# Performance work log

Measured on AMD Instinct MI355X. Metric: run time of the kernel, lower is better.

## Reference

```python
import jax, jax.numpy as jnp
import numpy as np

B, C, H, W = 8, 64, 256, 256
SQ = 256  # max(int(64*16*0.25),1)

def setup_inputs() -> dict:
    key = jax.random.key(0)
    k1, k2, k3, k4, k5 = jax.random.split(key, 5)
    t = jax.random.normal(k1, (B, C, H, W), dtype=jnp.float32)
    reduce_w = jax.random.normal(k2, (SQ, 16 * C), dtype=jnp.float32) * (1.0 / np.sqrt(16 * C))
    reduce_b = jax.random.normal(k3, (SQ,), dtype=jnp.float32) * 0.01
    expand_w = jax.random.normal(k4, (16 * C, SQ), dtype=jnp.float32) * (1.0 / np.sqrt(SQ))
    expand_b = jax.random.normal(k5, (16 * C,), dtype=jnp.float32) * 0.01
    return {"t": t, "reduce_w": reduce_w, "reduce_b": reduce_b,
            "expand_w": expand_w, "expand_b": expand_b}

def _mish(x):
    return x * jnp.tanh(jax.nn.softplus(x))

def reference(t, reduce_w, reduce_b, expand_w, expand_b):
    b, c, h, w = t.shape  # h, w assumed multiples of 4 (no pad needed)
    gh, gw = h // 4, w // 4
    # split into 4x4 grid of patches: [B, C, 4, gh, 4, gw]
    tg = t.reshape(b, c, 4, gh, 4, gw)
    # global avg pool per patch -> [B, C, 4, 4]; reorder to cat order (i*4+j)*C + c
    pooled = tg.mean(axis=(3, 5))                      # [B, C, 4, 4]
    pooled = pooled.transpose(0, 2, 3, 1).reshape(b, 16 * c)  # [B, 16C]
    # squeeze-excite MLP (1x1 convs on [B,16C,1,1] == linear layers)
    s = _mish(pooled @ reduce_w.T + reduce_b)          # [B, SQ]
    g = jax.nn.sigmoid(s @ expand_w.T + expand_b)      # [B, 16C]
    # gates back to grid: [B, 4, 4, C] -> [B, C, 4, 1, 4, 1]
    gates = g.reshape(b, 4, 4, c).transpose(0, 3, 1, 2)[:, :, :, None, :, None]
    out = (tg * gates).reshape(b, c, h, w)
    return out
```

## Files before the change

kernel.cpp:

```cpp
#include <hip/hip_runtime.h>
#include <math.h>


#define Bsz 8
#define Csz 64
#define Hsz 256
#define Wsz 256
#define SQsz 256
#define C16 1024

typedef float f32x4 __attribute__((ext_vector_type(4)));

__global__ __launch_bounds__(256) void pool_kernel(const float* __restrict__ t,
                                                   float* __restrict__ pooled) {
    int bid = blockIdx.x;
    int p   = bid & 15;
    int bc  = bid >> 4;
    int i   = p >> 2, j = p & 3;
    const float* base = t + (((size_t)bc * Hsz + (size_t)i * 64) * Wsz + (size_t)j * 64);
    int tid = threadIdx.x;
    float sum = 0.f;
#pragma unroll
    for (int k = 0; k < 4; ++k) {
        int g    = tid + k * 256;
        int row  = g >> 4;
        int col4 = g & 15;
        f32x4 v = *(const f32x4*)(base + (size_t)row * Wsz + col4 * 4);
        sum += v.x + v.y + v.z + v.w;
    }
#pragma unroll
    for (int off = 32; off > 0; off >>= 1) sum += __shfl_down(sum, off, 64);
    __shared__ float wsum[4];
    if ((tid & 63) == 0) wsum[tid >> 6] = sum;
    __syncthreads();
    if (tid == 0) {
        float s = wsum[0] + wsum[1] + wsum[2] + wsum[3];
        int b = bc >> 6;
        int c = bc & 63;
        pooled[b * C16 + p * Csz + c] = s * (1.0f / 4096.0f);
    }
}

__global__ __launch_bounds__(1024) void reduce_kernel(const float* __restrict__ pooled,
                                                      const float* __restrict__ reduce_w,
                                                      const float* __restrict__ reduce_b,
                                                      float* __restrict__ s_out) {
    int o   = blockIdx.x;
    int tid = threadIdx.x;
    int w   = tid >> 6;
    int l   = tid & 63;
    float wv = reduce_w[(size_t)o * C16 + tid];
    float acc[Bsz];
#pragma unroll
    for (int b = 0; b < Bsz; ++b)
        acc[b] = wv * pooled[b * C16 + tid];
#pragma unroll
    for (int off = 32; off > 0; off >>= 1) {
#pragma unroll
        for (int b = 0; b < Bsz; ++b)
            acc[b] += __shfl_xor(acc[b], off, 64);
    }
    __shared__ float red[16][Bsz];
    if (l == 0) {
#pragma unroll
        for (int b = 0; b < Bsz; ++b) red[w][b] = acc[b];
    }
    __syncthreads();
    if (tid < Bsz) {
        float x = reduce_b[o];
#pragma unroll
        for (int q = 0; q < 16; ++q) x += red[q][tid];
        float sp = (x > 15.f) ? x : log1pf(expf(x));
        s_out[tid * SQsz + o] = x * tanhf(sp);
    }
}

__global__ __launch_bounds__(256) void expand_kernel(const float* __restrict__ s_in,
                                                     const float* __restrict__ expand_w,
                                                     const float* __restrict__ expand_b,
                                                     float* __restrict__ g_out) {
    int o   = blockIdx.x;
    int tid = threadIdx.x;
    int w   = tid >> 6;
    int l   = tid & 63;
    float wv = expand_w[(size_t)o * SQsz + tid];
    float acc[Bsz];
#pragma unroll
    for (int b = 0; b < Bsz; ++b)
        acc[b] = wv * s_in[b * SQsz + tid];
#pragma unroll
    for (int off = 32; off > 0; off >>= 1) {
#pragma unroll
        for (int b = 0; b < Bsz; ++b)
            acc[b] += __shfl_xor(acc[b], off, 64);
    }
    __shared__ float red[4][Bsz];
    if (l == 0) {
#pragma unroll
        for (int b = 0; b < Bsz; ++b) red[w][b] = acc[b];
    }
    __syncthreads();
    if (tid < Bsz) {
        float x = expand_b[o] + red[0][tid] + red[1][tid] + red[2][tid] + red[3][tid];
        g_out[tid * C16 + o] = 1.0f / (1.0f + expf(-x));
    }
}

__global__ __launch_bounds__(256) void scale_kernel(const float* __restrict__ t,
                                                    const float* __restrict__ g,
                                                    float* __restrict__ out) {
    unsigned int idx = blockIdx.x * 256u + threadIdx.x;
    int w4 = idx & 63;
    int h  = (idx >> 6) & 255;
    int c  = (idx >> 14) & 63;
    int b  = idx >> 20;
    int p  = ((h >> 6) << 2) | (w4 >> 4);
    float gate = g[(b << 10) + (p << 6) + c];
    f32x4 v = __builtin_nontemporal_load((const f32x4*)(t + (size_t)idx * 4));
    f32x4 r;
    r.x = v.x * gate;
    r.y = v.y * gate;
    r.z = v.z * gate;
    r.w = v.w * gate;
    __builtin_nontemporal_store(r, (f32x4*)(out + (size_t)idx * 4));
}

extern "C" void kernel_launch(void* const* d_in, const int* in_sizes, int n_in,
                              void* d_out, int out_size, void* d_ws, size_t ws_size,
                              hipStream_t stream) {
    const float* t        = (const float*)d_in[0];
    const float* reduce_w = (const float*)d_in[1];
    const float* reduce_b = (const float*)d_in[2];
    const float* expand_w = (const float*)d_in[3];
    const float* expand_b = (const float*)d_in[4];
    float* out = (float*)d_out;

    float* pooled = (float*)d_ws;
    float* s_buf  = pooled + Bsz * C16;
    float* g_buf  = s_buf + Bsz * SQsz;

    pool_kernel  <<<Bsz * Csz * 16, 256, 0, stream>>>(t, pooled);
    reduce_kernel<<<SQsz,          1024, 0, stream>>>(pooled, reduce_w, reduce_b, s_buf);
    expand_kernel<<<C16,            256, 0, stream>>>(s_buf, expand_w, expand_b, g_buf);
    scale_kernel <<<32768,          256, 0, stream>>>(t, g_buf, out);
}
```

Measured before the change: 260.4 us.

## Fuse pool, SE MLP, and scale into one persistent kernel with grid barriers

Replaces the four separate kernel launches with a single persistent kernel of 512 blocks that synchronise through a hierarchical atomic grid barrier between the pool, reduce, expand and scale phases. Each block pools one full (b,c) plane, and the scale phase loops over strided chunks. The scale loads of t are now ordinary cached loads, so data read during pooling may be served from cache. The goal is to remove launch gaps and the separate pass over t. The cost is reliance on all 512 blocks being co-resident (2 per CU), plus barrier spin overhead and fewer blocks in flight during the streaming phases.

```diff
diff --git a/kernel.cpp b/kernel.cpp
--- a/kernel.cpp
+++ b/kernel.cpp
@@ -8,121 +8,162 @@
 #define Wsz 256
 #define SQsz 256
 #define C16 1024
+#define NBLK 512
 
 typedef float f32x4 __attribute__((ext_vector_type(4)));
 
-__global__ __launch_bounds__(256) void pool_kernel(const float* __restrict__ t,
-                                                   float* __restrict__ pooled) {
-    int bid = blockIdx.x;
-    int p   = bid & 15;
-    int bc  = bid >> 4;
-    int i   = p >> 2, j = p & 3;
-    const float* base = t + (((size_t)bc * Hsz + (size_t)i * 64) * Wsz + (size_t)j * 64);
-    int tid = threadIdx.x;
-    float sum = 0.f;
-#pragma unroll
-    for (int k = 0; k < 4; ++k) {
-        int g    = tid + k * 256;
-        int row  = g >> 4;
-        int col4 = g & 15;
-        f32x4 v = *(const f32x4*)(base + (size_t)row * Wsz + col4 * 4);
-        sum += v.x + v.y + v.z + v.w;
+__device__ __attribute__((aligned(128))) unsigned g_leaf[8][32];
+__device__ unsigned g_root = 0;
+__device__ unsigned g_gen  = 0;
+
+__device__ __forceinline__ void grid_barrier(int bid) {
+    __syncthreads();
+    if (threadIdx.x == 0) {
+        __threadfence();
+        unsigned g0 = __hip_atomic_load(&g_gen, __ATOMIC_ACQUIRE, __HIP_MEMORY_SCOPE_AGENT);
+        int leaf = bid & 7;
+        unsigned a = __hip_atomic_fetch_add(&g_leaf[leaf][0], 1u,
+                                            __ATOMIC_ACQ_REL, __HIP_MEMORY_SCOPE_AGENT);
+        bool last = false;
+        if (a == 63u) {
+            unsigned r = __hip_atomic_fetch_add(&g_root, 1u,
+                                                __ATOMIC_ACQ_REL, __HIP_MEMORY_SCOPE_AGENT);
+            if (r == 7u) {
+                for (int i = 0; i < 8; ++i)
+                    __hip_atomic_store(&g_leaf[i][0], 0u, __ATOMIC_RELAXED, __HIP_MEMORY_SCOPE_AGENT);
+                __hip_atomic_store(&g_root, 0u, __ATOMIC_RELAXED, __HIP_MEMORY_SCOPE_AGENT);
+                __hip_atomic_fetch_add(&g_gen, 1u, __ATOMIC_RELEASE, __HIP_MEMORY_SCOPE_AGENT);
+                last = true;
+            }
+        }
+        if (!last) {
+            while (__hip_atomic_load(&g_gen, __ATOMIC_ACQUIRE, __HIP_MEMORY_SCOPE_AGENT) == g0)
+                __builtin_amdgcn_s_sleep(2);
+        }
     }
-#pragma unroll
-    for (int off = 32; off > 0; off >>= 1) sum += __shfl_down(sum, off, 64);
-    __shared__ float wsum[4];
-    if ((tid & 63) == 0) wsum[tid >> 6] = sum;
     __syncthreads();
-    if (tid == 0) {
-        float s = wsum[0] + wsum[1] + wsum[2] + wsum[3];
-        int b = bc >> 6;
-        int c = bc & 63;
-        pooled[b * C16 + p * Csz + c] = s * (1.0f / 4096.0f);
-    }
 }
 
-__global__ __launch_bounds__(1024) void reduce_kernel(const float* __restrict__ pooled,
-                                                      const float* __restrict__ reduce_w,
-                                                      const float* __restrict__ reduce_b,
-                                                      float* __restrict__ s_out) {
-    int o   = blockIdx.x;
-    int tid = threadIdx.x;
-    int w   = tid >> 6;
-    int l   = tid & 63;
-    float wv = reduce_w[(size_t)o * C16 + tid];
-    float acc[Bsz];
+__global__ __launch_bounds__(256, 2) void fused_kernel(
+    const float* __restrict__ t,
+    const float* __restrict__ reduce_w,
+    const float* __restrict__ reduce_b,
+    const float* __restrict__ expand_w,
+    const float* __restrict__ expand_b,
+    float* __restrict__ out,
+    float* __restrict__ ws)
+{
+    float* pooled = ws;
+    float* s_buf  = ws + Bsz * C16;
+    float* g_buf  = s_buf + Bsz * SQsz;
+
+    const int bid  = blockIdx.x;
+    const int tid  = threadIdx.x;
+    const int lane = tid & 63;
+    const int wid  = tid >> 6;
+
+    {
+        const float* base = t + (size_t)bid * (Hsz * Wsz);
+        float a = 0.f;
+#pragma unroll 8
+        for (int r = 0; r < 64; ++r) {
+            f32x4 v = *(const f32x4*)(base + (size_t)(wid * 64 + r) * Wsz + lane * 4);
+            a += v.x + v.y + v.z + v.w;
+        }
 #pragma unroll
-    for (int b = 0; b < Bsz; ++b)
-        acc[b] = wv * pooled[b * C16 + tid];
+        for (int m = 8; m >= 1; m >>= 1) a += __shfl_xor(a, m, 64);
+        __shared__ float psum[4][4];
+        if ((lane & 15) == 0) psum[wid][lane >> 4] = a;
+        __syncthreads();
+        if (tid < 16) {
+            int b = bid >> 6, c = bid & 63;
+            pooled[b * C16 + tid * Csz + c] = psum[tid >> 2][tid & 3] * (1.0f / 4096.0f);
+        }
+    }
+    grid_barrier(bid);
+
+    if (bid < SQsz) {
+        const int o = bid;
+        f32x4 wv = ((const f32x4*)(reduce_w + (size_t)o * C16))[tid];
+        float acc[Bsz];
 #pragma unroll
-    for (int off = 32; off > 0; off >>= 1) {
+        for (int b = 0; b < Bsz; ++b) {
+            f32x4 pv = ((const f32x4*)pooled)[b * 256 + tid];
+            acc[b] = wv.x * pv.x + wv.y * pv.y + wv.z * pv.z + wv.w * pv.w;
+        }
 #pragma unroll
-        for (int b = 0; b < Bsz; ++b)
-            acc[b] += __shfl_xor(acc[b], off, 64);
+        for (int off = 32; off >= 1; off >>= 1) {
+#pragma unroll
+            for (int b = 0; b < Bsz; ++b)
+                acc[b] += __shfl_xor(acc[b], off, 64);
+        }
+        __shared__ float cr[4][8];
+        if (lane == 0) {
+#pragma unroll
+            for (int b = 0; b < Bsz; ++b) cr[wid][b] = acc[b];
+        }
+        __syncthreads();
+        if (tid < Bsz) {
+            float x = reduce_b[o] + cr[0][tid] + cr[1][tid] + cr[2][tid] + cr[3][tid];
+            float sp = (x > 15.f) ? x : log1pf(expf(x));
+            s_buf[tid * SQsz + o] = x * tanhf(sp);
+        }
     }
-    __shared__ float red[16][Bsz];
-    if (l == 0) {
+    grid_barrier(bid);
+
+    {
+        const int o0 = bid * 2, o1 = o0 + 1;
+        float wv0 = expand_w[(size_t)o0 * SQsz + tid];
+        float wv1 = expand_w[(size_t)o1 * SQsz + tid];
+        float acc0[Bsz], acc1[Bsz];
 #pragma unroll
-        for (int b = 0; b < Bsz; ++b) red[w][b] = acc[b];
+        for (int b = 0; b < Bsz; ++b) {
+            float sv = s_buf[b * SQsz + tid];
+            acc0[b] = wv0 * sv;
+            acc1[b] = wv1 * sv;
+        }
+#pragma unroll
+        for (int off = 32; off >= 1; off >>= 1) {
+#pragma unroll
+            for (int b = 0; b < Bsz; ++b) {
+                acc0[b] += __shfl_xor(acc0[b], off, 64);
+                acc1[b] += __shfl_xor(acc1[b], off, 64);
+            }
+        }
+        __shared__ float cr0[4][8], cr1[4][8];
+        if (lane == 0) {
+#pragma unroll
+            for (int b = 0; b < Bsz; ++b) { cr0[wid][b] = acc0[b]; cr1[wid][b] = acc1[b]; }
+        }
+        __syncthreads();
+        if (tid < Bsz) {
+            float x = expand_b[o0] + cr0[0][tid] + cr0[1][tid] + cr0[2][tid] + cr0[3][tid];
+            g_buf[tid * C16 + o0] = 1.0f / (1.0f + expf(-x));
+        } else if (tid >= 64 && tid < 64 + Bsz) {
+            int b = tid - 64;
+            float x = expand_b[o1] + cr1[0][b] + cr1[1][b] + cr1[2][b] + cr1[3][b];
+            g_buf[b * C16 + o1] = 1.0f / (1.0f + expf(-x));
+        }
     }
-    __syncthreads();
-    if (tid < Bsz) {
-        float x = reduce_b[o];
-#pragma unroll
-        for (int q = 0; q < 16; ++q) x += red[q][tid];
-        float sp = (x > 15.f) ? x : log1pf(expf(x));
-        s_out[tid * SQsz + o] = x * tanhf(sp);
+    grid_barrier(bid);
+
+#pragma unroll 8
+    for (int it = 0; it < 64; ++it) {
+        unsigned int idx = (unsigned int)(it * NBLK + bid) * 256u + tid;
+        int w4 = idx & 63;
+        int h  = (idx >> 6) & 255;
+        int c  = (idx >> 14) & 63;
+        int b  = idx >> 20;
+        int p  = ((h >> 6) << 2) | (w4 >> 4);
+        float gate = g_buf[(b << 10) + (p << 6) + c];
+        f32x4 v = *(const f32x4*)(t + (size_t)idx * 4);
+        f32x4 r;
+        r.x = v.x * gate;
+        r.y = v.y * gate;
+        r.z = v.z * gate;
+        r.w = v.w * gate;
+        __builtin_nontemporal_store(r, (f32x4*)(out + (size_t)idx * 4));
     }
-}
-
-__global__ __launch_bounds__(256) void expand_kernel(const float* __restrict__ s_in,
-                                                     const float* __restrict__ expand_w,
-                                                     const float* __restrict__ expand_b,
-                                                     float* __restrict__ g_out) {
-    int o   = blockIdx.x;
-    int tid = threadIdx.x;
-    int w   = tid >> 6;
-    int l   = tid & 63;
-    float wv = expand_w[(size_t)o * SQsz + tid];
-    float acc[Bsz];
-#pragma unroll
-    for (int b = 0; b < Bsz; ++b)
-        acc[b] = wv * s_in[b * SQsz + tid];
-#pragma unroll
-    for (int off = 32; off > 0; off >>= 1) {
-#pragma unroll
-        for (int b = 0; b < Bsz; ++b)
-            acc[b] += __shfl_xor(acc[b], off, 64);
-    }
-    __shared__ float red[4][Bsz];
-    if (l == 0) {
-#pragma unroll
-        for (int b = 0; b < Bsz; ++b) red[w][b] = acc[b];
-    }
-    __syncthreads();
-    if (tid < Bsz) {
-        float x = expand_b[o] + red[0][tid] + red[1][tid] + red[2][tid] + red[3][tid];
-        g_out[tid * C16 + o] = 1.0f / (1.0f + expf(-x));
-    }
-}
-
-__global__ __launch_bounds__(256) void scale_kernel(const float* __restrict__ t,
-                                                    const float* __restrict__ g,
-                                                    float* __restrict__ out) {
-    unsigned int idx = blockIdx.x * 256u + threadIdx.x;
-    int w4 = idx & 63;
-    int h  = (idx >> 6) & 255;
-    int c  = (idx >> 14) & 63;
-    int b  = idx >> 20;
-    int p  = ((h >> 6) << 2) | (w4 >> 4);
-    float gate = g[(b << 10) + (p << 6) + c];
-    f32x4 v = __builtin_nontemporal_load((const f32x4*)(t + (size_t)idx * 4));
-    f32x4 r;
-    r.x = v.x * gate;
-    r.y = v.y * gate;
-    r.z = v.z * gate;
-    r.w = v.w * gate;
-    __builtin_nontemporal_store(r, (f32x4*)(out + (size_t)idx * 4));
 }
 
 extern "C" void kernel_launch(void* const* d_in, const int* in_sizes, int n_in,
@@ -134,13 +175,8 @@
     const float* expand_w = (const float*)d_in[3];
     const float* expand_b = (const float*)d_in[4];
     float* out = (float*)d_out;
+    float* ws  = (float*)d_ws;
 
-    float* pooled = (float*)d_ws;
-    float* s_buf  = pooled + Bsz * C16;
-    float* g_buf  = s_buf + Bsz * SQsz;
-
-    pool_kernel  <<<Bsz * Csz * 16, 256, 0, stream>>>(t, pooled);
-    reduce_kernel<<<SQsz,          1024, 0, stream>>>(pooled, reduce_w, reduce_b, s_buf);
-    expand_kernel<<<C16,            256, 0, stream>>>(s_buf, expand_w, expand_b, g_buf);
-    scale_kernel <<<32768,          256, 0, stream>>>(t, g_buf, out);
+    fused_kernel<<<NBLK, 256, 0, stream>>>(t, reduce_w, reduce_b,
+                                           expand_w, expand_b, out, ws);
 }
```

New measurement: 402.3 us. 54.5% more time.
